# Performance work log

Measured on AMD Instinct MI355X. Metric: run time of the kernel, lower is better.

## Reference

```python
import jax, jax.numpy as jnp
import numpy as np

D_OUT = 10
N_BINS = 50
DELTA_SCALE = 60.0
TEMPERATURE = 1.0
CAND_BATCH = 1000  # hard-coded in the torch forward loop
EPS = 1e-8


def setup_inputs() -> dict:
    key = jax.random.key(0)
    ks = jax.random.split(key, 7)
    n_q, n_c, d_num, d_cat = 512, 8000, 6, 20
    return {
        "x_num": jax.random.normal(ks[0], (n_q, d_num), dtype=jnp.float32),
        "x_cat": jax.random.uniform(ks[1], (n_q, d_cat), dtype=jnp.float32),
        "candidate_x_num": jax.random.normal(ks[2], (n_c, d_num), dtype=jnp.float32),
        "candidate_x_cat": jax.random.uniform(ks[3], (n_c, d_cat), dtype=jnp.float32),
        "candidate_y": jax.random.randint(ks[4], (n_c,), 0, D_OUT, dtype=jnp.int64),
        # delta = rand(d_in_num, n_bins) * delta_scale (Parameter init)
        "delta": jax.random.uniform(ks[5], (d_num, N_BINS), dtype=jnp.float32) * DELTA_SCALE,
        # u = rand(d_in_num, n_bins) (buffer)
        "u": jax.random.uniform(ks[6], (d_num, N_BINS), dtype=jnp.float32),
    }


def _feature_map(x, delta, u):
    # x: [N, d_num] -> bin indices [N, d_num * n_bins]
    scaled_u = u * delta  # [d_num, n_bins]
    bins = jnp.ceil((x[:, :, None] - scaled_u[None]) / delta[None])
    return bins.reshape(x.shape[0], -1)


def reference(x_num, x_cat, candidate_x_num, candidate_x_cat, candidate_y, delta, u):
    x_enc = jnp.concatenate([_feature_map(x_num, delta, u), x_cat], axis=1)          # [Nq, D]
    c_enc = jnp.concatenate([_feature_map(candidate_x_num, delta, u), candidate_x_cat], axis=1)  # [Nc, D]
    y_oh = jax.nn.one_hot(candidate_y, D_OUT, dtype=jnp.float32)                     # [Nc, d_out]

    n_c, d = c_enc.shape
    n_chunks = n_c // CAND_BATCH
    c_chunks = c_enc.reshape(n_chunks, CAND_BATCH, d)
    y_chunks = y_oh.reshape(n_chunks, CAND_BATCH, D_OUT)

    def step(carry, batch):
        logits, lse = carry
        cx, cy = batch
        # L1 cdist: [Nq, CAND_BATCH]
        dist = jnp.sum(jnp.abs(x_enc[:, None, :] - cx[None, :, :]), axis=-1) / TEMPERATURE
        logits = logits + jnp.exp(-dist) @ cy
        # NOTE: faithful to torch code — per-batch logsumexp values are SUMMED
        lse = lse + jax.nn.logsumexp(-dist, axis=1)
        return (logits, lse), None

    n_q = x_enc.shape[0]
    init = (jnp.zeros((n_q, D_OUT), jnp.float32), jnp.zeros((n_q,), jnp.float32))
    (logits, lse), _ = jax.lax.scan(step, init, (c_chunks, y_chunks))
    return jnp.log(logits + EPS) - lse[:, None]
```

## Files before the change

kernel.cpp:

```cpp
#include <hip/hip_runtime.h>
#include <math.h>

#define NQ 512
#define NC 8000
#define DNUM 6
#define NBINS 50
#define DCAT 20
#define DENC 26
#define DOUT 10
#define CHUNK 1000
#define NCHUNK 8

__global__ void encode(const float* __restrict__ c_num, const float* __restrict__ c_cat,
                       const float* __restrict__ x_num, const float* __restrict__ x_cat,
                       const float* __restrict__ delta, const float* __restrict__ u,
                       float* __restrict__ cEnc, float* __restrict__ qEnc) {
    int i = blockIdx.x * 256 + threadIdx.x;
    const int nA = (NC + NQ) * DNUM;
    const int nB = (NC + NQ) * DCAT;
    if (i < nA) {
        int f = i % DNUM, p = i / DNUM;
        bool is_c = p < NC;
        int idx = is_c ? p : p - NC;
        float v = (is_c ? c_num : x_num)[idx * DNUM + f];
        float g = 0.f;
        for (int j = 0; j < NBINS; ++j) {
            float dl = delta[f * NBINS + j];
            float sc = u[f * NBINS + j] * dl;
            g += ceilf((v - sc) / dl);
        }
        if (is_c) cEnc[f * NC + idx] = g;
        else      qEnc[f * NQ + idx] = g;
    } else if (i < nA + nB) {
        int i2 = i - nA;
        int k = i2 % DCAT, p = i2 / DCAT;
        bool is_c = p < NC;
        int idx = is_c ? p : p - NC;
        float v = (is_c ? c_cat : x_cat)[idx * DCAT + k];
        if (is_c) cEnc[(DNUM + k) * NC + idx] = v;
        else      qEnc[(DNUM + k) * NQ + idx] = v;
    }
}

__global__ __launch_bounds__(512) void nca_all(
    const float* __restrict__ cEnc, const float* __restrict__ qEnc,
    const int* __restrict__ cy, float* __restrict__ out) {
    __shared__ float xs[DENC * 2];
    __shared__ float ms_parts[NCHUNK * 8 * 4];
    __shared__ float cls_parts[8][2 * DOUT];
    __shared__ float tmp[2][NCHUNK];
    __shared__ float lse_sh[2];

    const int tid = threadIdx.x;
    const int q0 = blockIdx.x * 2;
    if (tid < DENC * 2) {
        int d = tid >> 1, q = tid & 1;
        xs[tid] = qEnc[d * NQ + q0 + q];
    }
    __syncthreads();

    float xr0[DENC], xr1[DENC];
#pragma unroll
    for (int d = 0; d < DENC; ++d) { xr0[d] = xs[2 * d]; xr1[d] = xs[2 * d + 1]; }

    const bool act = tid < 500;
    const int cl = act ? 2 * tid : 996;
    const int lane = tid & 63, wave = tid >> 6;

    float cls[2 * DOUT];
#pragma unroll
    for (int k = 0; k < 2 * DOUT; ++k) cls[k] = 0.f;

    for (int chunk = 0; chunk < NCHUNK; ++chunk) {
        const float* cp = cEnc + chunk * CHUNK + cl;
        float2 cv[DENC];
#pragma unroll
        for (int d = 0; d < DENC; ++d) cv[d] = *(const float2*)(cp + (size_t)d * NC);

        float a00 = 0.f, a01 = 0.f, a10 = 0.f, a11 = 0.f;
#pragma unroll
        for (int d = 0; d < DENC; ++d) {
            a00 += fabsf(cv[d].x - xr0[d]); a01 += fabsf(cv[d].y - xr0[d]);
            a10 += fabsf(cv[d].x - xr1[d]); a11 += fabsf(cv[d].y - xr1[d]);
        }

        float m0 = act ? fminf(a00, a01) : INFINITY;
        float m1 = act ? fminf(a10, a11) : INFINITY;
#pragma unroll
        for (int sh = 32; sh >= 1; sh >>= 1) {
            m0 = fminf(m0, __shfl_xor(m0, sh));
            m1 = fminf(m1, __shfl_xor(m1, sh));
        }

        int2 y = *(const int2*)(cy + chunk * CHUNK + cl);
        float s0 = 0.f, s1 = 0.f;
        if (act) {
            float e00 = __expf(-a00), e01 = __expf(-a01);
            float e10 = __expf(-a10), e11 = __expf(-a11);
            s0 = __expf(m0 - a00) + __expf(m0 - a01);
            s1 = __expf(m1 - a10) + __expf(m1 - a11);
#pragma unroll
            for (int k = 0; k < DOUT; ++k) {
                cls[k]        += (y.x == k ? e00 : 0.f) + (y.y == k ? e01 : 0.f);
                cls[DOUT + k] += (y.x == k ? e10 : 0.f) + (y.y == k ? e11 : 0.f);
            }
        }
#pragma unroll
        for (int sh = 32; sh >= 1; sh >>= 1) {
            s0 += __shfl_xor(s0, sh);
            s1 += __shfl_xor(s1, sh);
        }
        if (lane == 0) {
            float* p = ms_parts + (chunk * 8 + wave) * 4;
            p[0] = m0; p[1] = s0; p[2] = m1; p[3] = s1;
        }
    }

#pragma unroll
    for (int k = 0; k < 2 * DOUT; ++k) {
#pragma unroll
        for (int sh = 32; sh >= 1; sh >>= 1) cls[k] += __shfl_xor(cls[k], sh);
    }
    if (lane == 0) {
#pragma unroll
        for (int k = 0; k < 2 * DOUT; ++k) cls_parts[wave][k] = cls[k];
    }
    __syncthreads();

    if (tid < 16) {
        int q = tid & 1, ch = tid >> 1;
        const float* p = ms_parts + ch * 32 + 2 * q;
        float M = INFINITY;
#pragma unroll
        for (int w = 0; w < 8; ++w) M = fminf(M, p[w * 4]);
        float S = 0.f;
#pragma unroll
        for (int w = 0; w < 8; ++w) S += __expf(M - p[w * 4]) * p[w * 4 + 1];
        tmp[q][ch] = logf(S) - M;
    }
    __syncthreads();
    if (tid < 2) {
        float l = 0.f;
#pragma unroll
        for (int ch = 0; ch < NCHUNK; ++ch) l += tmp[tid][ch];
        lse_sh[tid] = l;
    }
    __syncthreads();
    if (tid < 2 * DOUT) {
        int q = tid / DOUT, k = tid % DOUT;
        float s = 0.f;
#pragma unroll
        for (int w = 0; w < 8; ++w) s += cls_parts[w][q * DOUT + k];
        out[(q0 + q) * DOUT + k] = logf(s + 1e-8f) - lse_sh[q];
    }
}

extern "C" void kernel_launch(void* const* d_in, const int* in_sizes, int n_in,
                              void* d_out, int out_size, void* d_ws, size_t ws_size,
                              hipStream_t stream) {
    const float* x_num = (const float*)d_in[0];
    const float* x_cat = (const float*)d_in[1];
    const float* c_num = (const float*)d_in[2];
    const float* c_cat = (const float*)d_in[3];
    const int*   c_y   = (const int*)d_in[4];
    const float* delta = (const float*)d_in[5];
    const float* u     = (const float*)d_in[6];

    float* ws = (float*)d_ws;
    float* cEnc = ws;
    float* qEnc = cEnc + (size_t)DENC * NC;

    const int total = (NC + NQ) * DENC;
    encode<<<(total + 255) / 256, 256, 0, stream>>>(
        c_num, c_cat, x_num, x_cat, delta, u, cEnc, qEnc);
    nca_all<<<NQ / 2, 512, 0, stream>>>(cEnc, qEnc, c_y, (float*)d_out);
}
```

Measured before the change: 93.04 us.

## Fuse encode and NCA kernels via cooperative grid sync with double-buffered chunk loads

Merges the encoding kernel and the main distance/softmax kernel into one cooperative launch. A grid-stride encode phase is followed by a grid-wide sync, then the existing per-query-pair computation runs. The chunk loop is unrolled with two register buffers so the next chunk's loads are issued before the current chunk is computed, and the class accumulation is rewritten with fmaf masks. This removes one kernel launch and the gap between kernels, but adds grid-sync cost and register pressure that may reduce occupancy.

```diff
diff --git a/kernel.cpp b/kernel.cpp
--- a/kernel.cpp
+++ b/kernel.cpp
@@ -1,4 +1,5 @@
 #include <hip/hip_runtime.h>
+#include <hip/hip_cooperative_groups.h>
 #include <math.h>
 
 #define NQ 512
@@ -10,48 +11,56 @@
 #define DOUT 10
 #define CHUNK 1000
 #define NCHUNK 8
-
-__global__ void encode(const float* __restrict__ c_num, const float* __restrict__ c_cat,
-                       const float* __restrict__ x_num, const float* __restrict__ x_cat,
-                       const float* __restrict__ delta, const float* __restrict__ u,
-                       float* __restrict__ cEnc, float* __restrict__ qEnc) {
-    int i = blockIdx.x * 256 + threadIdx.x;
+#define NBLK 256
+#define NTHR 512
+#define GSIZE (NBLK * NTHR)
+
+__global__ __launch_bounds__(NTHR) void fused(
+    const float* __restrict__ c_num, const float* __restrict__ c_cat,
+    const float* __restrict__ x_num, const float* __restrict__ x_cat,
+    const float* __restrict__ delta, const float* __restrict__ u,
+    const int* __restrict__ cy,
+    float* __restrict__ cEnc, float* __restrict__ qEnc,
+    float* __restrict__ out) {
+
+    const int tid = threadIdx.x;
+    const int gtid = blockIdx.x * NTHR + tid;
+
     const int nA = (NC + NQ) * DNUM;
-    const int nB = (NC + NQ) * DCAT;
-    if (i < nA) {
-        int f = i % DNUM, p = i / DNUM;
-        bool is_c = p < NC;
-        int idx = is_c ? p : p - NC;
-        float v = (is_c ? c_num : x_num)[idx * DNUM + f];
-        float g = 0.f;
-        for (int j = 0; j < NBINS; ++j) {
-            float dl = delta[f * NBINS + j];
-            float sc = u[f * NBINS + j] * dl;
-            g += ceilf((v - sc) / dl);
+    const int nTot = nA + (NC + NQ) * DCAT;
+    for (int i = gtid; i < nTot; i += GSIZE) {
+        if (i < nA) {
+            int f = i % DNUM, p = i / DNUM;
+            bool is_c = p < NC;
+            int idx = is_c ? p : p - NC;
+            float v = (is_c ? c_num : x_num)[idx * DNUM + f];
+            float g = 0.f;
+            for (int j = 0; j < NBINS; ++j) {
+                float dl = delta[f * NBINS + j];
+                float sc = u[f * NBINS + j] * dl;
+                g += ceilf((v - sc) / dl);
+            }
+            if (is_c) cEnc[f * NC + idx] = g;
+            else      qEnc[f * NQ + idx] = g;
+        } else {
+            int i2 = i - nA;
+            int k = i2 % DCAT, p = i2 / DCAT;
+            bool is_c = p < NC;
+            int idx = is_c ? p : p - NC;
+            float v = (is_c ? c_cat : x_cat)[idx * DCAT + k];
+            if (is_c) cEnc[(DNUM + k) * NC + idx] = v;
+            else      qEnc[(DNUM + k) * NQ + idx] = v;
         }
-        if (is_c) cEnc[f * NC + idx] = g;
-        else      qEnc[f * NQ + idx] = g;
-    } else if (i < nA + nB) {
-        int i2 = i - nA;
-        int k = i2 % DCAT, p = i2 / DCAT;
-        bool is_c = p < NC;
-        int idx = is_c ? p : p - NC;
-        float v = (is_c ? c_cat : x_cat)[idx * DCAT + k];
-        if (is_c) cEnc[(DNUM + k) * NC + idx] = v;
-        else      qEnc[(DNUM + k) * NQ + idx] = v;
-    }
-}
-
-__global__ __launch_bounds__(512) void nca_all(
-    const float* __restrict__ cEnc, const float* __restrict__ qEnc,
-    const int* __restrict__ cy, float* __restrict__ out) {
+    }
+    __threadfence();
+    cooperative_groups::this_grid().sync();
+
     __shared__ float xs[DENC * 2];
     __shared__ float ms_parts[NCHUNK * 8 * 4];
     __shared__ float cls_parts[8][2 * DOUT];
     __shared__ float tmp[2][NCHUNK];
     __shared__ float lse_sh[2];
 
-    const int tid = threadIdx.x;
     const int q0 = blockIdx.x * 2;
     if (tid < DENC * 2) {
         int d = tid >> 1, q = tid & 1;
@@ -71,50 +80,66 @@
 #pragma unroll
     for (int k = 0; k < 2 * DOUT; ++k) cls[k] = 0.f;
 
-    for (int chunk = 0; chunk < NCHUNK; ++chunk) {
-        const float* cp = cEnc + chunk * CHUNK + cl;
-        float2 cv[DENC];
-#pragma unroll
-        for (int d = 0; d < DENC; ++d) cv[d] = *(const float2*)(cp + (size_t)d * NC);
-
-        float a00 = 0.f, a01 = 0.f, a10 = 0.f, a11 = 0.f;
-#pragma unroll
-        for (int d = 0; d < DENC; ++d) {
-            a00 += fabsf(cv[d].x - xr0[d]); a01 += fabsf(cv[d].y - xr0[d]);
-            a10 += fabsf(cv[d].x - xr1[d]); a11 += fabsf(cv[d].y - xr1[d]);
-        }
-
-        float m0 = act ? fminf(a00, a01) : INFINITY;
-        float m1 = act ? fminf(a10, a11) : INFINITY;
-#pragma unroll
-        for (int sh = 32; sh >= 1; sh >>= 1) {
-            m0 = fminf(m0, __shfl_xor(m0, sh));
-            m1 = fminf(m1, __shfl_xor(m1, sh));
-        }
-
-        int2 y = *(const int2*)(cy + chunk * CHUNK + cl);
-        float s0 = 0.f, s1 = 0.f;
-        if (act) {
-            float e00 = __expf(-a00), e01 = __expf(-a01);
-            float e10 = __expf(-a10), e11 = __expf(-a11);
-            s0 = __expf(m0 - a00) + __expf(m0 - a01);
-            s1 = __expf(m1 - a10) + __expf(m1 - a11);
-#pragma unroll
-            for (int k = 0; k < DOUT; ++k) {
-                cls[k]        += (y.x == k ? e00 : 0.f) + (y.y == k ? e01 : 0.f);
-                cls[DOUT + k] += (y.x == k ? e10 : 0.f) + (y.y == k ? e11 : 0.f);
-            }
-        }
-#pragma unroll
-        for (int sh = 32; sh >= 1; sh >>= 1) {
-            s0 += __shfl_xor(s0, sh);
-            s1 += __shfl_xor(s1, sh);
-        }
-        if (lane == 0) {
-            float* p = ms_parts + (chunk * 8 + wave) * 4;
-            p[0] = m0; p[1] = s0; p[2] = m1; p[3] = s1;
-        }
-    }
+    float2 bufA[DENC], bufB[DENC];
+
+#define LOADC(BUF, CH) do {                                                   \
+    const float* _p = cEnc + (CH) * CHUNK + cl;                               \
+    _Pragma("unroll")                                                         \
+    for (int d = 0; d < DENC; ++d)                                            \
+        BUF[d] = *(const float2*)(_p + (size_t)d * NC);                       \
+} while (0)
+
+#define COMPUTE(BUF, CH) do {                                                 \
+    int2 y = *(const int2*)(cy + (CH) * CHUNK + cl);                          \
+    float a00 = 0.f, a01 = 0.f, a10 = 0.f, a11 = 0.f;         \
+    _Pragma("unroll")                                                         \
+    for (int d = 0; d < DENC; ++d) {                                          \
+        a00 += fabsf(BUF[d].x - xr0[d]); a01 += fabsf(BUF[d].y - xr0[d]);     \
+        a10 += fabsf(BUF[d].x - xr1[d]); a11 += fabsf(BUF[d].y - xr1[d]);     \
+    }                                                                         \
+    float m0 = act ? fminf(a00, a01) : INFINITY;                              \
+    float m1 = act ? fminf(a10, a11) : INFINITY;                              \
+    _Pragma("unroll")                                                         \
+    for (int sh = 32; sh >= 1; sh >>= 1) {                                    \
+        m0 = fminf(m0, __shfl_xor(m0, sh));                                   \
+        m1 = fminf(m1, __shfl_xor(m1, sh));                                   \
+    }                                                                         \
+    float s0 = 0.f, s1 = 0.f;                                                 \
+    if (act) {                                                                \
+        float e00 = __expf(-a00), e01 = __expf(-a01);                         \
+        float e10 = __expf(-a10), e11 = __expf(-a11);                         \
+        s0 = __expf(m0 - a00) + __expf(m0 - a01);                             \
+        s1 = __expf(m1 - a10) + __expf(m1 - a11);                             \
+        _Pragma("unroll")                                                     \
+        for (int k = 0; k < DOUT; ++k) {                                      \
+                       \
+            float mx = (y.x == k) ? 1.f : 0.f;                                \
+            float my = (y.y == k) ? 1.f : 0.f;                                \
+            cls[k]        = fmaf(mx, e00, fmaf(my, e01, cls[k]));             \
+            cls[DOUT + k] = fmaf(mx, e10, fmaf(my, e11, cls[DOUT + k]));      \
+        }                                                                     \
+    }                                                                         \
+    _Pragma("unroll")                                                         \
+    for (int sh = 32; sh >= 1; sh >>= 1) {                                    \
+        s0 += __shfl_xor(s0, sh);                                             \
+        s1 += __shfl_xor(s1, sh);                                             \
+    }                                                                         \
+    if (lane == 0) {                                                          \
+        float* _q = ms_parts + ((CH) * 8 + wave) * 4;                         \
+        _q[0] = m0; _q[1] = s0; _q[2] = m1; _q[3] = s1;                       \
+    }                                                                         \
+} while (0)
+
+    LOADC(bufA, 0);
+#pragma unroll
+    for (int cc = 0; cc < NCHUNK; cc += 2) {
+        LOADC(bufB, cc + 1);
+        COMPUTE(bufA, cc);
+        if (cc + 2 < NCHUNK) LOADC(bufA, cc + 2);
+        COMPUTE(bufB, cc + 1);
+    }
+#undef LOADC
+#undef COMPUTE
 
 #pragma unroll
     for (int k = 0; k < 2 * DOUT; ++k) {
@@ -169,9 +194,13 @@
     float* ws = (float*)d_ws;
     float* cEnc = ws;
     float* qEnc = cEnc + (size_t)DENC * NC;
-
-    const int total = (NC + NQ) * DENC;
-    encode<<<(total + 255) / 256, 256, 0, stream>>>(
-        c_num, c_cat, x_num, x_cat, delta, u, cEnc, qEnc);
-    nca_all<<<NQ / 2, 512, 0, stream>>>(cEnc, qEnc, c_y, (float*)d_out);
+    float* outp = (float*)d_out;
+
+    void* args[] = {
+        (void*)&c_num, (void*)&c_cat, (void*)&x_num, (void*)&x_cat,
+        (void*)&delta, (void*)&u, (void*)&c_y,
+        (void*)&cEnc, (void*)&qEnc, (void*)&outp
+    };
+    hipLaunchCooperativeKernel(reinterpret_cast<const void*>(&fused),
+                               dim3(NBLK), dim3(NTHR), args, 0u, stream);
 }
```

After: 195.5 us. 110% more time.

## Split candidate chunks across two blocks per query pair with atomic last-block merge

Applied to the files above, without the earlier changes.

Each query pair is now handled by two blocks, each covering half of the candidate chunks. Partial class sums and log-sum-exp values go to a workspace, and the second block to arrive (found with an atomic counter) combines them into the output. This doubles the grid from 256 to 512 blocks to fill more compute units. It also loads candidate features in two halves to cut register pressure, adds an occupancy hint in launch bounds, and rewrites the one-hot accumulation as FMAs. The cost is extra partial writes, fences and atomics, plus counter resets folded into the encode kernel.

```diff
diff --git a/kernel.cpp b/kernel.cpp
--- a/kernel.cpp
+++ b/kernel.cpp
@@ -10,12 +10,17 @@
 #define DOUT 10
 #define CHUNK 1000
 #define NCHUNK 8
+#define NQP 256
+#define CPH 4
+#define PPITCH 24
 
 __global__ void encode(const float* __restrict__ c_num, const float* __restrict__ c_cat,
                        const float* __restrict__ x_num, const float* __restrict__ x_cat,
                        const float* __restrict__ delta, const float* __restrict__ u,
-                       float* __restrict__ cEnc, float* __restrict__ qEnc) {
+                       float* __restrict__ cEnc, float* __restrict__ qEnc,
+                       int* __restrict__ counters) {
     int i = blockIdx.x * 256 + threadIdx.x;
+    if (i < NQP) counters[i] = 0;
     const int nA = (NC + NQ) * DNUM;
     const int nB = (NC + NQ) * DCAT;
     if (i < nA) {
@@ -42,17 +47,22 @@
     }
 }
 
-__global__ __launch_bounds__(512) void nca_all(
+__global__ __launch_bounds__(512, 4) void nca_half(
     const float* __restrict__ cEnc, const float* __restrict__ qEnc,
-    const int* __restrict__ cy, float* __restrict__ out) {
+    const int* __restrict__ cy, float* __restrict__ pPart,
+    int* __restrict__ counters, float* __restrict__ out) {
     __shared__ float xs[DENC * 2];
-    __shared__ float ms_parts[NCHUNK * 8 * 4];
+    __shared__ float ms_parts[CPH * 8 * 4];
     __shared__ float cls_parts[8][2 * DOUT];
-    __shared__ float tmp[2][NCHUNK];
+    __shared__ float tmp[2][CPH];
     __shared__ float lse_sh[2];
+    __shared__ int amLast;
 
     const int tid = threadIdx.x;
-    const int q0 = blockIdx.x * 2;
+    const int qp = blockIdx.x >> 1;
+    const int half = blockIdx.x & 1;
+    const int q0 = qp * 2;
+
     if (tid < DENC * 2) {
         int d = tid >> 1, q = tid & 1;
         xs[tid] = qEnc[d * NQ + q0 + q];
@@ -71,17 +81,25 @@
 #pragma unroll
     for (int k = 0; k < 2 * DOUT; ++k) cls[k] = 0.f;
 
-    for (int chunk = 0; chunk < NCHUNK; ++chunk) {
-        const float* cp = cEnc + chunk * CHUNK + cl;
-        float2 cv[DENC];
-#pragma unroll
-        for (int d = 0; d < DENC; ++d) cv[d] = *(const float2*)(cp + (size_t)d * NC);
-
+    for (int lc = 0; lc < CPH; ++lc) {
+        const int c = half * CPH + lc;
+        const float* cp = cEnc + (size_t)c * CHUNK + cl;
         float a00 = 0.f, a01 = 0.f, a10 = 0.f, a11 = 0.f;
-#pragma unroll
-        for (int d = 0; d < DENC; ++d) {
+
+        float2 cv[13];
+#pragma unroll
+        for (int d = 0; d < 13; ++d) cv[d] = *(const float2*)(cp + (size_t)d * NC);
+#pragma unroll
+        for (int d = 0; d < 13; ++d) {
             a00 += fabsf(cv[d].x - xr0[d]); a01 += fabsf(cv[d].y - xr0[d]);
             a10 += fabsf(cv[d].x - xr1[d]); a11 += fabsf(cv[d].y - xr1[d]);
+        }
+#pragma unroll
+        for (int d = 0; d < 13; ++d) cv[d] = *(const float2*)(cp + (size_t)(13 + d) * NC);
+#pragma unroll
+        for (int d = 0; d < 13; ++d) {
+            a00 += fabsf(cv[d].x - xr0[13 + d]); a01 += fabsf(cv[d].y - xr0[13 + d]);
+            a10 += fabsf(cv[d].x - xr1[13 + d]); a11 += fabsf(cv[d].y - xr1[13 + d]);
         }
 
         float m0 = act ? fminf(a00, a01) : INFINITY;
@@ -92,7 +110,7 @@
             m1 = fminf(m1, __shfl_xor(m1, sh));
         }
 
-        int2 y = *(const int2*)(cy + chunk * CHUNK + cl);
+        int2 y = *(const int2*)(cy + (size_t)c * CHUNK + cl);
         float s0 = 0.f, s1 = 0.f;
         if (act) {
             float e00 = __expf(-a00), e01 = __expf(-a01);
@@ -101,8 +119,10 @@
             s1 = __expf(m1 - a10) + __expf(m1 - a11);
 #pragma unroll
             for (int k = 0; k < DOUT; ++k) {
-                cls[k]        += (y.x == k ? e00 : 0.f) + (y.y == k ? e01 : 0.f);
-                cls[DOUT + k] += (y.x == k ? e10 : 0.f) + (y.y == k ? e11 : 0.f);
+                float mx = (y.x == k) ? 1.f : 0.f;
+                float my = (y.y == k) ? 1.f : 0.f;
+                cls[k]        = fmaf(mx, e00, fmaf(my, e01, cls[k]));
+                cls[DOUT + k] = fmaf(mx, e10, fmaf(my, e11, cls[DOUT + k]));
             }
         }
 #pragma unroll
@@ -111,7 +131,7 @@
             s1 += __shfl_xor(s1, sh);
         }
         if (lane == 0) {
-            float* p = ms_parts + (chunk * 8 + wave) * 4;
+            float* p = ms_parts + (lc * 8 + wave) * 4;
             p[0] = m0; p[1] = s0; p[2] = m1; p[3] = s1;
         }
     }
@@ -127,7 +147,7 @@
     }
     __syncthreads();
 
-    if (tid < 16) {
+    if (tid < 2 * CPH) {
         int q = tid & 1, ch = tid >> 1;
         const float* p = ms_parts + ch * 32 + 2 * q;
         float M = INFINITY;
@@ -142,16 +162,33 @@
     if (tid < 2) {
         float l = 0.f;
 #pragma unroll
-        for (int ch = 0; ch < NCHUNK; ++ch) l += tmp[tid][ch];
+        for (int ch = 0; ch < CPH; ++ch) l += tmp[tid][ch];
         lse_sh[tid] = l;
     }
     __syncthreads();
+
+    float* myPart = pPart + (size_t)(qp * 2 + half) * PPITCH;
     if (tid < 2 * DOUT) {
-        int q = tid / DOUT, k = tid % DOUT;
         float s = 0.f;
 #pragma unroll
-        for (int w = 0; w < 8; ++w) s += cls_parts[w][q * DOUT + k];
-        out[(q0 + q) * DOUT + k] = logf(s + 1e-8f) - lse_sh[q];
+        for (int w = 0; w < 8; ++w) s += cls_parts[w][tid];
+        myPart[tid] = s;
+    }
+    if (tid == 20 || tid == 21) myPart[tid] = lse_sh[tid - 20];
+    __threadfence();
+    __syncthreads();
+    if (tid == 0) amLast = (atomicAdd(&counters[qp], 1) == 1);
+    __syncthreads();
+    if (amLast) {
+        __threadfence();
+        if (tid < 2 * DOUT) {
+            int q = tid / DOUT, k = tid % DOUT;
+            const float* pa = pPart + (size_t)(qp * 2) * PPITCH;
+            const float* pb = pPart + (size_t)(qp * 2 + 1) * PPITCH;
+            float s = pa[tid] + pb[tid];
+            float l = pa[20 + q] + pb[20 + q];
+            out[(q0 + q) * DOUT + k] = logf(s + 1e-8f) - l;
+        }
     }
 }
 
@@ -169,9 +206,12 @@
     float* ws = (float*)d_ws;
     float* cEnc = ws;
     float* qEnc = cEnc + (size_t)DENC * NC;
+    float* pPart = qEnc + (size_t)DENC * NQ;
+    int*   counters = (int*)(pPart + (size_t)NQP * 2 * PPITCH);
 
     const int total = (NC + NQ) * DENC;
     encode<<<(total + 255) / 256, 256, 0, stream>>>(
-        c_num, c_cat, x_num, x_cat, delta, u, cEnc, qEnc);
-    nca_all<<<NQ / 2, 512, 0, stream>>>(cEnc, qEnc, c_y, (float*)d_out);
+        c_num, c_cat, x_num, x_cat, delta, u, cEnc, qEnc, counters);
+    nca_half<<<NQP * 2, 512, 0, stream>>>(cEnc, qEnc, c_y, pPart, counters,
+                                          (float*)d_out);
 }
```

After: 246.1 us. +164.5%, slower.

## Process four queries per block and split candidates across block pairs with last-block merge

Applied to the files above, without the earlier changes.

Each block now handles four queries against half of every candidate chunk, where it previously handled two queries against whole chunks. The two halves write partial class sums and per-chunk (min, sum) pairs to workspace. An atomic counter picks the last-arriving block, which merges both halves and writes the output. This doubles the reuse of each candidate load across queries while keeping 256 blocks. The cost is more query registers, a global partial buffer, threadfence/atomic synchronisation, and counters that the encode kernel must reset on every launch.

```diff
diff --git a/kernel.cpp b/kernel.cpp
--- a/kernel.cpp
+++ b/kernel.cpp
@@ -10,12 +10,18 @@
 #define DOUT 10
 #define CHUNK 1000
 #define NCHUNK 8
+#define NQUAD 128
+#define QPB 4
+#define CPH 500
+#define PPITCH 104
 
 __global__ void encode(const float* __restrict__ c_num, const float* __restrict__ c_cat,
                        const float* __restrict__ x_num, const float* __restrict__ x_cat,
                        const float* __restrict__ delta, const float* __restrict__ u,
-                       float* __restrict__ cEnc, float* __restrict__ qEnc) {
+                       float* __restrict__ cEnc, float* __restrict__ qEnc,
+                       int* __restrict__ counters) {
     int i = blockIdx.x * 256 + threadIdx.x;
+    if (i < NQUAD) counters[i] = 0;
     const int nA = (NC + NQ) * DNUM;
     const int nB = (NC + NQ) * DCAT;
     if (i < nA) {
@@ -42,116 +48,133 @@
     }
 }
 
-__global__ __launch_bounds__(512) void nca_all(
+__global__ __launch_bounds__(512) void nca_quad(
     const float* __restrict__ cEnc, const float* __restrict__ qEnc,
-    const int* __restrict__ cy, float* __restrict__ out) {
-    __shared__ float xs[DENC * 2];
-    __shared__ float ms_parts[NCHUNK * 8 * 4];
-    __shared__ float cls_parts[8][2 * DOUT];
-    __shared__ float tmp[2][NCHUNK];
-    __shared__ float lse_sh[2];
+    const int* __restrict__ cy, float* __restrict__ pPart,
+    int* __restrict__ counters, float* __restrict__ out) {
+    __shared__ float ms_parts[NCHUNK][8][2 * QPB];
+    __shared__ float cls_parts[8][QPB * DOUT];
+    __shared__ int amLast;
 
     const int tid = threadIdx.x;
-    const int q0 = blockIdx.x * 2;
-    if (tid < DENC * 2) {
-        int d = tid >> 1, q = tid & 1;
-        xs[tid] = qEnc[d * NQ + q0 + q];
+    const int quad = blockIdx.x >> 1;
+    const int half = blockIdx.x & 1;
+    const int q0 = quad * QPB;
+
+    float xr[QPB][DENC];
+#pragma unroll
+    for (int q = 0; q < QPB; ++q)
+#pragma unroll
+        for (int d = 0; d < DENC; ++d)
+            xr[q][d] = qEnc[d * NQ + q0 + q];
+
+    const bool act = tid < CPH;
+    const int cidx = half * CPH + (act ? tid : CPH - 1);
+    const int lane = tid & 63, wave = tid >> 6;
+
+    float cls[QPB * DOUT];
+#pragma unroll
+    for (int k = 0; k < QPB * DOUT; ++k) cls[k] = 0.f;
+
+    for (int ch = 0; ch < NCHUNK; ++ch) {
+        const float* cp = cEnc + (size_t)ch * CHUNK + cidx;
+        float a[QPB] = {0.f, 0.f, 0.f, 0.f};
+#pragma unroll
+        for (int d = 0; d < DENC; ++d) {
+            float c = cp[(size_t)d * NC];
+#pragma unroll
+            for (int q = 0; q < QPB; ++q) a[q] += fabsf(c - xr[q][d]);
+        }
+
+        float m[QPB];
+#pragma unroll
+        for (int q = 0; q < QPB; ++q) m[q] = act ? a[q] : INFINITY;
+#pragma unroll
+        for (int sh = 32; sh >= 1; sh >>= 1)
+#pragma unroll
+            for (int q = 0; q < QPB; ++q) m[q] = fminf(m[q], __shfl_xor(m[q], sh));
+
+        int y = cy[(size_t)ch * CHUNK + cidx];
+        float s[QPB] = {0.f, 0.f, 0.f, 0.f};
+        if (act) {
+#pragma unroll
+            for (int q = 0; q < QPB; ++q) {
+                float e = __expf(-a[q]);
+                s[q] = __expf(m[q] - a[q]);
+#pragma unroll
+                for (int k = 0; k < DOUT; ++k) {
+                    float mk = (y == k) ? 1.f : 0.f;
+                    cls[q * DOUT + k] = fmaf(mk, e, cls[q * DOUT + k]);
+                }
+            }
+        }
+#pragma unroll
+        for (int sh = 32; sh >= 1; sh >>= 1)
+#pragma unroll
+            for (int q = 0; q < QPB; ++q) s[q] += __shfl_xor(s[q], sh);
+        if (lane == 0) {
+#pragma unroll
+            for (int q = 0; q < QPB; ++q) {
+                ms_parts[ch][wave][q * 2]     = m[q];
+                ms_parts[ch][wave][q * 2 + 1] = s[q];
+            }
+        }
+    }
+
+#pragma unroll
+    for (int k = 0; k < QPB * DOUT; ++k)
+#pragma unroll
+        for (int sh = 32; sh >= 1; sh >>= 1) cls[k] += __shfl_xor(cls[k], sh);
+    if (lane == 0) {
+#pragma unroll
+        for (int k = 0; k < QPB * DOUT; ++k) cls_parts[wave][k] = cls[k];
     }
     __syncthreads();
 
-    float xr0[DENC], xr1[DENC];
-#pragma unroll
-    for (int d = 0; d < DENC; ++d) { xr0[d] = xs[2 * d]; xr1[d] = xs[2 * d + 1]; }
-
-    const bool act = tid < 500;
-    const int cl = act ? 2 * tid : 996;
-    const int lane = tid & 63, wave = tid >> 6;
-
-    float cls[2 * DOUT];
-#pragma unroll
-    for (int k = 0; k < 2 * DOUT; ++k) cls[k] = 0.f;
-
-    for (int chunk = 0; chunk < NCHUNK; ++chunk) {
-        const float* cp = cEnc + chunk * CHUNK + cl;
-        float2 cv[DENC];
-#pragma unroll
-        for (int d = 0; d < DENC; ++d) cv[d] = *(const float2*)(cp + (size_t)d * NC);
-
-        float a00 = 0.f, a01 = 0.f, a10 = 0.f, a11 = 0.f;
-#pragma unroll
-        for (int d = 0; d < DENC; ++d) {
-            a00 += fabsf(cv[d].x - xr0[d]); a01 += fabsf(cv[d].y - xr0[d]);
-            a10 += fabsf(cv[d].x - xr1[d]); a11 += fabsf(cv[d].y - xr1[d]);
-        }
-
-        float m0 = act ? fminf(a00, a01) : INFINITY;
-        float m1 = act ? fminf(a10, a11) : INFINITY;
-#pragma unroll
-        for (int sh = 32; sh >= 1; sh >>= 1) {
-            m0 = fminf(m0, __shfl_xor(m0, sh));
-            m1 = fminf(m1, __shfl_xor(m1, sh));
-        }
-
-        int2 y = *(const int2*)(cy + chunk * CHUNK + cl);
-        float s0 = 0.f, s1 = 0.f;
-        if (act) {
-            float e00 = __expf(-a00), e01 = __expf(-a01);
-            float e10 = __expf(-a10), e11 = __expf(-a11);
-            s0 = __expf(m0 - a00) + __expf(m0 - a01);
-            s1 = __expf(m1 - a10) + __expf(m1 - a11);
-#pragma unroll
-            for (int k = 0; k < DOUT; ++k) {
-                cls[k]        += (y.x == k ? e00 : 0.f) + (y.y == k ? e01 : 0.f);
-                cls[DOUT + k] += (y.x == k ? e10 : 0.f) + (y.y == k ? e11 : 0.f);
+    float* myPart = pPart + (size_t)(quad * 2 + half) * PPITCH;
+
+    if (tid < NCHUNK * QPB) {
+        int ch = tid >> 2, q = tid & 3;
+        float M = INFINITY;
+#pragma unroll
+        for (int w = 0; w < 8; ++w) M = fminf(M, ms_parts[ch][w][q * 2]);
+        float S = 0.f;
+#pragma unroll
+        for (int w = 0; w < 8; ++w)
+            S += __expf(M - ms_parts[ch][w][q * 2]) * ms_parts[ch][w][q * 2 + 1];
+        myPart[QPB * DOUT + ch * 8 + q * 2]     = M;
+        myPart[QPB * DOUT + ch * 8 + q * 2 + 1] = S;
+    }
+    if (tid < QPB * DOUT) {
+        float sum = 0.f;
+#pragma unroll
+        for (int w = 0; w < 8; ++w) sum += cls_parts[w][tid];
+        myPart[tid] = sum;
+    }
+    __threadfence();
+    __syncthreads();
+    if (tid == 0) amLast = (atomicAdd(&counters[quad], 1) == 1);
+    __syncthreads();
+    if (amLast) {
+        __threadfence();
+        if (tid < QPB * DOUT) {
+            int q = tid / DOUT, k = tid % DOUT;
+            const float* pa = pPart + (size_t)(quad * 2) * PPITCH;
+            const float* pb = pPart + (size_t)(quad * 2 + 1) * PPITCH;
+            float sum = pa[tid] + pb[tid];
+            float l = 0.f;
+#pragma unroll
+            for (int ch = 0; ch < NCHUNK; ++ch) {
+                float mA = pa[QPB * DOUT + ch * 8 + q * 2];
+                float sA = pa[QPB * DOUT + ch * 8 + q * 2 + 1];
+                float mB = pb[QPB * DOUT + ch * 8 + q * 2];
+                float sB = pb[QPB * DOUT + ch * 8 + q * 2 + 1];
+                float M = fminf(mA, mB);
+                float S = __expf(M - mA) * sA + __expf(M - mB) * sB;
+                l += logf(S) - M;
             }
-        }
-#pragma unroll
-        for (int sh = 32; sh >= 1; sh >>= 1) {
-            s0 += __shfl_xor(s0, sh);
-            s1 += __shfl_xor(s1, sh);
-        }
-        if (lane == 0) {
-            float* p = ms_parts + (chunk * 8 + wave) * 4;
-            p[0] = m0; p[1] = s0; p[2] = m1; p[3] = s1;
-        }
-    }
-
-#pragma unroll
-    for (int k = 0; k < 2 * DOUT; ++k) {
-#pragma unroll
-        for (int sh = 32; sh >= 1; sh >>= 1) cls[k] += __shfl_xor(cls[k], sh);
-    }
-    if (lane == 0) {
-#pragma unroll
-        for (int k = 0; k < 2 * DOUT; ++k) cls_parts[wave][k] = cls[k];
-    }
-    __syncthreads();
-
-    if (tid < 16) {
-        int q = tid & 1, ch = tid >> 1;
-        const float* p = ms_parts + ch * 32 + 2 * q;
-        float M = INFINITY;
-#pragma unroll
-        for (int w = 0; w < 8; ++w) M = fminf(M, p[w * 4]);
-        float S = 0.f;
-#pragma unroll
-        for (int w = 0; w < 8; ++w) S += __expf(M - p[w * 4]) * p[w * 4 + 1];
-        tmp[q][ch] = logf(S) - M;
-    }
-    __syncthreads();
-    if (tid < 2) {
-        float l = 0.f;
-#pragma unroll
-        for (int ch = 0; ch < NCHUNK; ++ch) l += tmp[tid][ch];
-        lse_sh[tid] = l;
-    }
-    __syncthreads();
-    if (tid < 2 * DOUT) {
-        int q = tid / DOUT, k = tid % DOUT;
-        float s = 0.f;
-#pragma unroll
-        for (int w = 0; w < 8; ++w) s += cls_parts[w][q * DOUT + k];
-        out[(q0 + q) * DOUT + k] = logf(s + 1e-8f) - lse_sh[q];
+            out[(q0 + q) * DOUT + k] = logf(sum + 1e-8f) - l;
+        }
     }
 }
 
@@ -169,9 +192,12 @@
     float* ws = (float*)d_ws;
     float* cEnc = ws;
     float* qEnc = cEnc + (size_t)DENC * NC;
+    float* pPart = qEnc + (size_t)DENC * NQ;
+    int*   counters = (int*)(pPart + (size_t)NQUAD * 2 * PPITCH);
 
     const int total = (NC + NQ) * DENC;
     encode<<<(total + 255) / 256, 256, 0, stream>>>(
-        c_num, c_cat, x_num, x_cat, delta, u, cEnc, qEnc);
-    nca_all<<<NQ / 2, 512, 0, stream>>>(cEnc, qEnc, c_y, (float*)d_out);
+        c_num, c_cat, x_num, x_cat, delta, u, cEnc, qEnc, counters);
+    nca_quad<<<NQUAD * 2, 512, 0, stream>>>(cEnc, qEnc, c_y, pPart, counters,
+                                            (float*)d_out);
 }
```

Measured after the change: 151.6 us. 1.63x slower.
